# Kernel tuning notes

Hardware: AMD Instinct MI355X
Metric: run time of the kernel (lower is better)

The kernel has to match this reference:

```python
import jax, jax.numpy as jnp
import numpy as np
from math import sqrt

B, S, D_MODEL, H, DK, DV = 8, 1024, 1024, 16, 64, 64
LN_EPS = 1e-5

def setup_inputs() -> dict:
    key = jax.random.key(0)
    ks = jax.random.split(key, 12)
    scale = 1.0 / sqrt(D_MODEL)
    return {
        "input_Q": jax.random.normal(ks[0], (B, S, D_MODEL), jnp.float32),
        "input_K": jax.random.normal(ks[1], (B, S, D_MODEL), jnp.float32),
        "input_V": jax.random.normal(ks[2], (B, S, D_MODEL), jnp.float32),
        "attn_mask": jax.random.randint(ks[3], (B, S, S), 0, 2).astype(bool),
        "matrix": jax.random.uniform(ks[4], (B, 1, S, S), jnp.float32),
        "Wq": jax.random.normal(ks[5], (D_MODEL, H * DK), jnp.float32) * scale,
        "Wk": jax.random.normal(ks[6], (D_MODEL, H * DK), jnp.float32) * scale,
        "Wv": jax.random.normal(ks[7], (D_MODEL, H * DV), jnp.float32) * scale,
        "Wfc": jax.random.normal(ks[8], (H * DV, D_MODEL), jnp.float32) * scale,
        "gamma": jnp.ones((D_MODEL,), jnp.float32),
        "beta": jnp.zeros((D_MODEL,), jnp.float32),
    }

def reference(input_Q, input_K, input_V, attn_mask, matrix, Wq, Wk, Wv, Wfc, gamma, beta):
    b, s, _ = input_Q.shape
    # QKV projections -> [b, h, s, d]
    Q = (input_Q @ Wq).reshape(b, s, H, DK).transpose(0, 2, 1, 3)
    K = (input_K @ Wk).reshape(b, s, H, DK).transpose(0, 2, 1, 3)
    V = (input_V @ Wv).reshape(b, s, H, DV).transpose(0, 2, 1, 3)
    scores = jnp.einsum('bhqd,bhkd->bhqk', Q, K) / sqrt(DK)
    scores = scores * matrix  # custom bias multiply, broadcast over heads
    scores = jnp.where(attn_mask[:, None, :, :], jnp.float32(-1e9), scores)
    attn = jax.nn.softmax(scores, axis=-1)  # dropout p=0 (eval)
    context = jnp.einsum('bhqk,bhkd->bhqd', attn, V)
    context = context.transpose(0, 2, 1, 3).reshape(b, s, H * DV)
    out = context @ Wfc
    mu = jnp.mean(out, axis=-1, keepdims=True)
    var = jnp.var(out, axis=-1, keepdims=True)
    return (out - mu) / jnp.sqrt(var + LN_EPS) * gamma + beta
```

## Files before the change

### kernel.cpp

```cpp
#include <hip/hip_runtime.h>
#include <hip/hip_bf16.h>

typedef __attribute__((ext_vector_type(8))) short short8;
typedef __attribute__((ext_vector_type(4))) float f32x4;

#define NH 16
#define SEQ 1024
#define DMODEL 1024
#define HD 64

__device__ __forceinline__ unsigned short f2bf(float f) {
  unsigned u = __builtin_bit_cast(unsigned, f);
  unsigned r = (u + 0x7FFFu + ((u >> 16) & 1u)) >> 16;
  return (unsigned short)r;
}

__device__ __forceinline__ void gld16(const unsigned short* g, unsigned short* l) {
  __builtin_amdgcn_global_load_lds(
      (const __attribute__((address_space(1))) unsigned int*)g,
      (__attribute__((address_space(3))) unsigned int*)l, 16, 0, 0);
}

__device__ __forceinline__ void stage_tile_gld(const unsigned short* __restrict__ gtile,
                                               unsigned short* ldsbuf, int w, int l) {
#pragma unroll
  for (int it = 0; it < 2; ++it) {
    int e = (w * 2 + it) * 512 + l * 8;
    int row = e >> 5, col = e & 31;
    gld16(gtile + (size_t)row * 1024 + col, ldsbuf + e);
  }
}

__global__ void mask_detect(const unsigned char* __restrict__ mask,
                            int* __restrict__ flag) {
  __shared__ int cA, cB;
  if (threadIdx.x == 0) { cA = 0; cB = 0; }
  __syncthreads();
  int a = 0, b = 0;
  for (int i = threadIdx.x; i < 4096; i += 256) {
    unsigned char v = mask[i];
    if (v) { if ((i & 3) == 0) a = 1; else b = 1; }
  }
  if (a) atomicOr(&cA, 1);
  if (b) atomicOr(&cB, 1);
  __syncthreads();
  if (threadIdx.x == 0) flag[0] = cA ? (cB ? 0 : 1) : 2;
}

__device__ __forceinline__ unsigned nib_of(int mmode,
    const unsigned char* __restrict__ mask, const int* __restrict__ maski,
    const float* __restrict__ maskf, size_t eoff) {
  if (mmode == 0) {
    unsigned mu = *(const unsigned*)(mask + eoff);
    return ((mu & 0xFFu) ? 1u : 0u) | ((mu & 0xFF00u) ? 2u : 0u) |
           ((mu & 0xFF0000u) ? 4u : 0u) | ((mu & 0xFF000000u) ? 8u : 0u);
  } else if (mmode == 1) {
    int4 m4 = *(const int4*)(maski + eoff);
    return (m4.x ? 1u : 0u) | (m4.y ? 2u : 0u) | (m4.z ? 4u : 0u) | (m4.w ? 8u : 0u);
  } else {
    float4 m4 = *(const float4*)(maskf + eoff);
    return (m4.x != 0.f ? 1u : 0u) | (m4.y != 0.f ? 2u : 0u) |
           (m4.z != 0.f ? 4u : 0u) | (m4.w != 0.f ? 8u : 0u);
  }
}

__global__ __launch_bounds__(256) void wtrans_kernel(
    const float* __restrict__ W0, const float* __restrict__ W1,
    const float* __restrict__ W2, const float* __restrict__ W3,
    unsigned short* __restrict__ out) {
  int z = blockIdx.z;
  const float* W = (z == 0) ? W0 : (z == 1) ? W1 : (z == 2) ? W2 : W3;
  unsigned short* o = out + (size_t)z * DMODEL * DMODEL;
  __shared__ float t[32][33];
  int tid = threadIdx.x;
  int tx = tid & 31, ty = tid >> 5;
  int n0 = blockIdx.x * 32, k0 = blockIdx.y * 32;
#pragma unroll
  for (int i = 0; i < 4; ++i)
    t[ty + 8 * i][tx] = W[(size_t)(k0 + ty + 8 * i) * DMODEL + n0 + tx];
  __syncthreads();
#pragma unroll
  for (int i = 0; i < 4; ++i)
    o[(size_t)(n0 + ty + 8 * i) * DMODEL + k0 + tx] = f2bf(t[tx][ty + 8 * i]);
}

__global__ __launch_bounds__(256) void cvt_bf16(
    const float* __restrict__ inQ, const float* __restrict__ inK,
    const float* __restrict__ inV, unsigned short* __restrict__ Abf) {
  int z = blockIdx.y;
  const float* src = (z == 0) ? inQ : (z == 1) ? inK : inV;
  unsigned short* dst = Abf + (size_t)z * 8192 * DMODEL;
  float scale = (z == 0) ? 0.125f : 1.0f;
  size_t i = ((size_t)blockIdx.x * 256 + threadIdx.x) * 8;
  float4 v0 = *(const float4*)&src[i];
  float4 v1 = *(const float4*)&src[i + 4];
  short8 r;
  r[0] = (short)f2bf(v0.x * scale); r[1] = (short)f2bf(v0.y * scale);
  r[2] = (short)f2bf(v0.z * scale); r[3] = (short)f2bf(v0.w * scale);
  r[4] = (short)f2bf(v1.x * scale); r[5] = (short)f2bf(v1.y * scale);
  r[6] = (short)f2bf(v1.z * scale); r[7] = (short)f2bf(v1.w * scale);
  *(short8*)&dst[i] = r;
}

__device__ __forceinline__ size_t kf_idx(int bh, int s, int d) {
  int kt = s >> 6, sl = s & 63;
  int lane = ((d >> 3) & 3) * 16 + (sl & 15);
  return ((size_t)bh * 16 + kt) * 4096 + ((((d >> 5) << 2) + (sl >> 4)) << 9) + lane * 8 + (d & 7);
}
__device__ __forceinline__ size_t vf_idx(int bh, int s, int d) {
  int kt = s >> 6, sl = s & 63;
  int lane = ((sl >> 3) & 3) * 16 + (d & 15);
  return ((size_t)bh * 16 + kt) * 4096 + ((((sl >> 5) << 2) + (d >> 4)) << 9) + lane * 8 + (sl & 7);
}

__global__ __launch_bounds__(256) void qkv_gemm_bf(
    const unsigned short* __restrict__ Abf, const unsigned short* __restrict__ Wt,
    unsigned short* __restrict__ Qp, unsigned short* __restrict__ Kf,
    unsigned short* __restrict__ Vf) {
  __shared__ unsigned short As[2][4096];
  __shared__ unsigned short Bs[2][4096];
  int tid = threadIdx.x;
  int which = blockIdx.z;
  const unsigned short* A = Abf + (size_t)which * 8192 * DMODEL;
  const unsigned short* Bt = Wt + (size_t)which * DMODEL * DMODEL;
  int m0 = blockIdx.x * 128, n0 = blockIdx.y * 128;
  int w = tid >> 6, l = tid & 63, lr = l & 15, lh = l >> 4;
  int wr = (w >> 1) * 64, wc = (w & 1) * 64;

  f32x4 acc[4][4];
#pragma unroll
  for (int i = 0; i < 4; ++i)
#pragma unroll
    for (int j = 0; j < 4; ++j) acc[i][j] = (f32x4){0.f, 0.f, 0.f, 0.f};

  const unsigned short* Abase = A + (size_t)m0 * DMODEL;
  const unsigned short* Bbase = Bt + (size_t)n0 * DMODEL;

  stage_tile_gld(Abase, As[0], w, l);
  stage_tile_gld(Bbase, Bs[0], w, l);
  __syncthreads();

  for (int kt = 0; kt < 32; ++kt) {
    int buf = kt & 1;
    if (kt < 31) {
      stage_tile_gld(Abase + (kt + 1) * 32, As[buf ^ 1], w, l);
      stage_tile_gld(Bbase + (kt + 1) * 32, Bs[buf ^ 1], w, l);
    }
    short8 a[4], b[4];
#pragma unroll
    for (int i = 0; i < 4; ++i) a[i] = *(const short8*)&As[buf][(wr + i * 16 + lr) * 32 + lh * 8];
#pragma unroll
    for (int i = 0; i < 4; ++i) b[i] = *(const short8*)&Bs[buf][(wc + i * 16 + lr) * 32 + lh * 8];
#pragma unroll
    for (int mi = 0; mi < 4; ++mi)
#pragma unroll
      for (int ni = 0; ni < 4; ++ni)
        acc[mi][ni] = __builtin_amdgcn_mfma_f32_16x16x32_bf16(a[mi], b[ni], acc[mi][ni], 0, 0, 0);
    __syncthreads();
  }

#pragma unroll
  for (int mi = 0; mi < 4; ++mi)
#pragma unroll
    for (int ni = 0; ni < 4; ++ni)
#pragma unroll
      for (int r = 0; r < 4; ++r) {
        int m = m0 + wr + mi * 16 + lh * 4 + r;
        int n = n0 + wc + ni * 16 + lr;
        int bb = m >> 10, s = m & 1023, hh = n >> 6, d = n & 63;
        int bh = bb * NH + hh;
        unsigned short val = f2bf(acc[mi][ni][r]);
        if (which == 0)      Qp[((size_t)bh * SEQ + s) * HD + d] = val;
        else if (which == 1) Kf[kf_idx(bh, s, d)] = val;
        else                 Vf[vf_idx(bh, s, d)] = val;
      }
}

__global__ __launch_bounds__(256) void qkv_gemm_legacy(
    const float* __restrict__ inQ, const float* __restrict__ inK,
    const float* __restrict__ inV, const unsigned short* __restrict__ Wt,
    unsigned short* __restrict__ Qp, unsigned short* __restrict__ Kf,
    unsigned short* __restrict__ Vf) {
  __shared__ unsigned short As[2][128][40];
  __shared__ unsigned short Bs[2][128][40];
  int tid = threadIdx.x;
  int which = blockIdx.z;
  const float* A = (which == 0) ? inQ : (which == 1) ? inK : inV;
  const unsigned short* Bt = Wt + (size_t)which * DMODEL * DMODEL;
  float scale = (which == 0) ? 0.125f : 1.0f;
  int m0 = blockIdx.x * 128, n0 = blockIdx.y * 128;
  int w = tid >> 6, l = tid & 63, lr = l & 15, lh = l >> 4;
  int wr = (w >> 1) * 64, wc = (w & 1) * 64;

  f32x4 acc[4][4];
#pragma unroll
  for (int i = 0; i < 4; ++i)
#pragma unroll
    for (int j = 0; j < 4; ++j) acc[i][j] = (f32x4){0.f, 0.f, 0.f, 0.f};

  const float* Abase = A + (size_t)m0 * DMODEL;
  const unsigned short* Bbase = Bt + (size_t)n0 * DMODEL;

  {
    int row = tid >> 1, seg = (tid & 1) << 4;
    const float4* p = (const float4*)(Abase + (size_t)row * DMODEL + seg);
    float4 v0 = p[0], v1 = p[1], v2 = p[2], v3 = p[3];
    short8 r0, r1;
    r0[0] = (short)f2bf(v0.x); r0[1] = (short)f2bf(v0.y);
    r0[2] = (short)f2bf(v0.z); r0[3] = (short)f2bf(v0.w);
    r0[4] = (short)f2bf(v1.x); r0[5] = (short)f2bf(v1.y);
    r0[6] = (short)f2bf(v1.z); r0[7] = (short)f2bf(v1.w);
    r1[0] = (short)f2bf(v2.x); r1[1] = (short)f2bf(v2.y);
    r1[2] = (short)f2bf(v2.z); r1[3] = (short)f2bf(v2.w);
    r1[4] = (short)f2bf(v3.x); r1[5] = (short)f2bf(v3.y);
    r1[6] = (short)f2bf(v3.z); r1[7] = (short)f2bf(v3.w);
    *(short8*)&As[0][row][seg] = r0;
    *(short8*)&As[0][row][seg + 8] = r1;
    const short8* pb = (const short8*)(Bbase + (size_t)row * DMODEL + seg);
    *(short8*)&Bs[0][row][seg] = pb[0];
    *(short8*)&Bs[0][row][seg + 8] = pb[1];
  }
  __syncthreads();

  for (int kt = 0; kt < 32; ++kt) {
    int buf = kt & 1;
    if (kt < 31) {
      int row = tid >> 1, seg = (tid & 1) << 4;
      const float4* p = (const float4*)(Abase + (kt + 1) * 32 + (size_t)row * DMODEL + seg);
      float4 v0 = p[0], v1 = p[1], v2 = p[2], v3 = p[3];
      short8 r0, r1;
      r0[0] = (short)f2bf(v0.x); r0[1] = (short)f2bf(v0.y);
      r0[2] = (short)f2bf(v0.z); r0[3] = (short)f2bf(v0.w);
      r0[4] = (short)f2bf(v1.x); r0[5] = (short)f2bf(v1.y);
      r0[6] = (short)f2bf(v1.z); r0[7] = (short)f2bf(v1.w);
      r1[0] = (short)f2bf(v2.x); r1[1] = (short)f2bf(v2.y);
      r1[2] = (short)f2bf(v2.z); r1[3] = (short)f2bf(v2.w);
      r1[4] = (short)f2bf(v3.x); r1[5] = (short)f2bf(v3.y);
      r1[6] = (short)f2bf(v3.z); r1[7] = (short)f2bf(v3.w);
      *(short8*)&As[buf ^ 1][row][seg] = r0;
      *(short8*)&As[buf ^ 1][row][seg + 8] = r1;
      const short8* pb = (const short8*)(Bbase + (kt + 1) * 32 + (size_t)row * DMODEL + seg);
      *(short8*)&Bs[buf ^ 1][row][seg] = pb[0];
      *(short8*)&Bs[buf ^ 1][row][seg + 8] = pb[1];
    }
    short8 a[4], b[4];
#pragma unroll
    for (int i = 0; i < 4; ++i) a[i] = *(const short8*)&As[buf][wr + i * 16 + lr][lh * 8];
#pragma unroll
    for (int i = 0; i < 4; ++i) b[i] = *(const short8*)&Bs[buf][wc + i * 16 + lr][lh * 8];
#pragma unroll
    for (int mi = 0; mi < 4; ++mi)
#pragma unroll
      for (int ni = 0; ni < 4; ++ni)
        acc[mi][ni] = __builtin_amdgcn_mfma_f32_16x16x32_bf16(a[mi], b[ni], acc[mi][ni], 0, 0, 0);
    __syncthreads();
  }

#pragma unroll
  for (int mi = 0; mi < 4; ++mi)
#pragma unroll
    for (int ni = 0; ni < 4; ++ni)
#pragma unroll
      for (int r = 0; r < 4; ++r) {
        int m = m0 + wr + mi * 16 + lh * 4 + r;
        int n = n0 + wc + ni * 16 + lr;
        int bb = m >> 10, s = m & 1023, hh = n >> 6, d = n & 63;
        int bh = bb * NH + hh;
        unsigned short val = f2bf(acc[mi][ni][r] * scale);
        if (which == 0)      Qp[((size_t)bh * SEQ + s) * HD + d] = val;
        else if (which == 1) Kf[kf_idx(bh, s, d)] = val;
        else                 Vf[vf_idx(bh, s, d)] = val;
      }
}

__global__ __launch_bounds__(512, 2) void attn_kernel(
    const unsigned short* __restrict__ Qp, const unsigned short* __restrict__ Kf,
    const unsigned short* __restrict__ Vf, const float* __restrict__ matrix,
    const unsigned char* __restrict__ mask, const int* __restrict__ maskmode,
    unsigned short* __restrict__ ctx) {
  __shared__ float Msc[2][32][68];
  __shared__ float Msb[2][32][68];
  __shared__ unsigned short Ps[8][16][72];

  int tid = threadIdx.x, w = tid >> 6, l = tid & 63, lr = l & 15, lh = l >> 4;
  int id = blockIdx.x;
  int b = id & 7;
  int rest = id >> 3;
  int qt = rest & 31, pass = rest >> 5;
  int q0 = qt * 32;
  int h = pass * 8 + w;
  int mmode = maskmode[0];
  const int* maski = (const int*)mask;
  const float* maskf = (const float*)mask;

  int srow = tid >> 4, sf4 = tid & 15;
  size_t mrow = ((size_t)b * SEQ + q0 + srow) * SEQ;

  int bh = b * NH + h;
  const unsigned short* Qb = Qp + (size_t)bh * SEQ * HD;
  size_t fb = (size_t)bh * 16 * 4096;

  short8 aq[2][2];
#pragma unroll
  for (int qs = 0; qs < 2; ++qs)
#pragma unroll
    for (int kd = 0; kd < 2; ++kd)
      aq[qs][kd] = *(const short8*)&Qb[(size_t)(q0 + qs * 16 + lr) * HD + kd * 32 + lh * 8];

  float lrun[2] = {0.f, 0.f};
  f32x4 cacc[2][4];
#pragma unroll
  for (int qs = 0; qs < 2; ++qs)
#pragma unroll
    for (int di = 0; di < 4; ++di) cacc[qs][di] = (f32x4){0.f, 0.f, 0.f, 0.f};

  {
    size_t eoff = mrow + sf4 * 4;
    float4 m0v = *(const float4*)&matrix[eoff];
    unsigned nb = nib_of(mmode, mask, maski, maskf, eoff);
    float4 sv, bsv;
    sv.x = (nb & 1u) ? 0.f : m0v.x;  bsv.x = (nb & 1u) ? -30000.f : -12.f;
    sv.y = (nb & 2u) ? 0.f : m0v.y;  bsv.y = (nb & 2u) ? -30000.f : -12.f;
    sv.z = (nb & 4u) ? 0.f : m0v.z;  bsv.z = (nb & 4u) ? -30000.f : -12.f;
    sv.w = (nb & 8u) ? 0.f : m0v.w;  bsv.w = (nb & 8u) ? -30000.f : -12.f;
    *(float4*)&Msc[0][srow][sf4 * 4] = sv;
    *(float4*)&Msb[0][srow][sf4 * 4] = bsv;
  }
  __syncthreads();

  int cur = 0;
  for (int kt = 0; kt < 16; ++kt) {
    float4 mpre = {0.f, 0.f, 0.f, 0.f};
    unsigned npre = 0;
    if (kt < 15) {
      size_t eoff = mrow + kt * 64 + 64 + sf4 * 4;
      mpre = *(const float4*)&matrix[eoff];
      npre = nib_of(mmode, mask, maski, maskf, eoff);
    }
    size_t ktb = fb + (size_t)kt * 4096;
    short8 bk[4][2], bv[4][2];
#pragma unroll
    for (int ni = 0; ni < 4; ++ni)
#pragma unroll
      for (int kd = 0; kd < 2; ++kd)
        bk[ni][kd] = *(const short8*)&Kf[ktb + (((kd << 2) + ni) << 9) + (l << 3)];
#pragma unroll
    for (int di = 0; di < 4; ++di)
#pragma unroll
      for (int kd = 0; kd < 2; ++kd)
        bv[di][kd] = *(const short8*)&Vf[ktb + (((kd << 2) + di) << 9) + (l << 3)];

#pragma unroll
    for (int qs = 0; qs < 2; ++qs) {
      f32x4 sc[4];
#pragma unroll
      for (int ni = 0; ni < 4; ++ni) sc[ni] = (f32x4){0.f, 0.f, 0.f, 0.f};
#pragma unroll
      for (int ni = 0; ni < 4; ++ni)
#pragma unroll
        for (int kd = 0; kd < 2; ++kd)
          sc[ni] = __builtin_amdgcn_mfma_f32_16x16x32_bf16(bk[ni][kd], aq[qs][kd], sc[ni], 0, 0, 0);
      int qrw = qs * 16 + lr;
      float psum = 0.f;
#pragma unroll
      for (int ni = 0; ni < 4; ++ni) {
        float4 sa = *(const float4*)&Msc[cur][qrw][(ni * 4 + lh) * 4];
        float4 sb = *(const float4*)&Msb[cur][qrw][(ni * 4 + lh) * 4];
        float p0 = __expf(sc[ni][0] * sa.x + sb.x);
        float p1 = __expf(sc[ni][1] * sa.y + sb.y);
        float p2 = __expf(sc[ni][2] * sa.z + sb.z);
        float p3 = __expf(sc[ni][3] * sa.w + sb.w);
        psum += (p0 + p1) + (p2 + p3);
        Ps[w][lr][ni * 16 + lh * 4 + 0] = f2bf(p0);
        Ps[w][lr][ni * 16 + lh * 4 + 1] = f2bf(p1);
        Ps[w][lr][ni * 16 + lh * 4 + 2] = f2bf(p2);
        Ps[w][lr][ni * 16 + lh * 4 + 3] = f2bf(p3);
      }
      lrun[qs] += psum;
      short8 ap[2];
#pragma unroll
      for (int kd = 0; kd < 2; ++kd)
        ap[kd] = *(const short8*)&Ps[w][lr][kd * 32 + lh * 8];
#pragma unroll
      for (int di = 0; di < 4; ++di)
#pragma unroll
        for (int kd = 0; kd < 2; ++kd)
          cacc[qs][di] = __builtin_amdgcn_mfma_f32_16x16x32_bf16(ap[kd], bv[di][kd], cacc[qs][di], 0, 0, 0);
    }
    if (kt < 15) {
      float4 sv, bsv;
      sv.x = (npre & 1u) ? 0.f : mpre.x;  bsv.x = (npre & 1u) ? -30000.f : -12.f;
      sv.y = (npre & 2u) ? 0.f : mpre.y;  bsv.y = (npre & 2u) ? -30000.f : -12.f;
      sv.z = (npre & 4u) ? 0.f : mpre.z;  bsv.z = (npre & 4u) ? -30000.f : -12.f;
      sv.w = (npre & 8u) ? 0.f : mpre.w;  bsv.w = (npre & 8u) ? -30000.f : -12.f;
      *(float4*)&Msc[cur ^ 1][srow][sf4 * 4] = sv;
      *(float4*)&Msb[cur ^ 1][srow][sf4 * 4] = bsv;
    }
    __syncthreads();
    cur ^= 1;
  }

#pragma unroll
  for (int qs = 0; qs < 2; ++qs) {
    float l2 = lrun[qs];
    l2 += __shfl_xor(l2, 16);
    l2 += __shfl_xor(l2, 32);
    float ls[4];
    int cbase = lh * 4;
#pragma unroll
    for (int r = 0; r < 4; ++r) ls[r] = __shfl(l2, cbase + r);
#pragma unroll
    for (int di = 0; di < 4; ++di)
#pragma unroll
      for (int r = 0; r < 4; ++r) {
        int q = q0 + qs * 16 + lh * 4 + r;
        int col = h * HD + di * 16 + lr;
        ctx[((size_t)b * SEQ + q) * DMODEL + col] = f2bf(cacc[qs][di][r] / ls[r]);
      }
  }
}

__global__ __launch_bounds__(256) void fc_gemm(
    const unsigned short* __restrict__ Actx, const unsigned short* __restrict__ Bt,
    float* __restrict__ Cout) {
  __shared__ unsigned short As[2][4096];
  __shared__ unsigned short Bs[2][4096];
  int tid = threadIdx.x;
  int m0 = blockIdx.x * 128, n0 = blockIdx.y * 128;
  int w = tid >> 6, l = tid & 63, lr = l & 15, lh = l >> 4;
  int wr = (w >> 1) * 64, wc = (w & 1) * 64;

  f32x4 acc[4][4];
#pragma unroll
  for (int i = 0; i < 4; ++i)
#pragma unroll
    for (int j = 0; j < 4; ++j) acc[i][j] = (f32x4){0.f, 0.f, 0.f, 0.f};

  const unsigned short* Abase = Actx + (size_t)m0 * DMODEL;
  const unsigned short* Bbase = Bt + (size_t)n0 * DMODEL;

  stage_tile_gld(Abase, As[0], w, l);
  stage_tile_gld(Bbase, Bs[0], w, l);
  __syncthreads();

  for (int kt = 0; kt < 32; ++kt) {
    int buf = kt & 1;
    if (kt < 31) {
      stage_tile_gld(Abase + (kt + 1) * 32, As[buf ^ 1], w, l);
      stage_tile_gld(Bbase + (kt + 1) * 32, Bs[buf ^ 1], w, l);
    }
    short8 a[4], b[4];
#pragma unroll
    for (int i = 0; i < 4; ++i) a[i] = *(const short8*)&As[buf][(wr + i * 16 + lr) * 32 + lh * 8];
#pragma unroll
    for (int i = 0; i < 4; ++i) b[i] = *(const short8*)&Bs[buf][(wc + i * 16 + lr) * 32 + lh * 8];
#pragma unroll
    for (int mi = 0; mi < 4; ++mi)
#pragma unroll
      for (int ni = 0; ni < 4; ++ni)
        acc[mi][ni] = __builtin_amdgcn_mfma_f32_16x16x32_bf16(a[mi], b[ni], acc[mi][ni], 0, 0, 0);
    __syncthreads();
  }

#pragma unroll
  for (int mi = 0; mi < 4; ++mi)
#pragma unroll
    for (int ni = 0; ni < 4; ++ni)
#pragma unroll
      for (int r = 0; r < 4; ++r) {
        int m = m0 + wr + mi * 16 + lh * 4 + r;
        int n = n0 + wc + ni * 16 + lr;
        Cout[(size_t)m * DMODEL + n] = acc[mi][ni][r];
      }
}

__global__ __launch_bounds__(256) void ln_kernel(
    const float* __restrict__ x, const float* __restrict__ gamma,
    const float* __restrict__ beta, float* __restrict__ out) {
  int row = blockIdx.x, tid = threadIdx.x;
  const float* xr = x + (size_t)row * DMODEL;
  float4 v = *(const float4*)&xr[tid * 4];
  float s = v.x + v.y + v.z + v.w;
  float s2 = v.x * v.x + v.y * v.y + v.z * v.z + v.w * v.w;
#pragma unroll
  for (int mm = 1; mm < 64; mm <<= 1) {
    s += __shfl_xor(s, mm);
    s2 += __shfl_xor(s2, mm);
  }
  __shared__ float red[8];
  int w = tid >> 6, l = tid & 63;
  if (l == 0) { red[w] = s; red[4 + w] = s2; }
  __syncthreads();
  s = red[0] + red[1] + red[2] + red[3];
  s2 = red[4] + red[5] + red[6] + red[7];
  float mu = s * (1.0f / 1024.0f);
  float var = s2 * (1.0f / 1024.0f) - mu * mu;
  float rstd = rsqrtf(var + 1e-5f);
  float4 g = *(const float4*)&gamma[tid * 4];
  float4 be = *(const float4*)&beta[tid * 4];
  float4 o;
  o.x = (v.x - mu) * rstd * g.x + be.x;
  o.y = (v.y - mu) * rstd * g.y + be.y;
  o.z = (v.z - mu) * rstd * g.z + be.z;
  o.w = (v.w - mu) * rstd * g.w + be.w;
  *(float4*)(out + (size_t)row * DMODEL + tid * 4) = o;
}

extern "C" void kernel_launch(void* const* d_in, const int* in_sizes, int n_in,
                              void* d_out, int out_size, void* d_ws, size_t ws_size,
                              hipStream_t stream) {
  const float* inQ = (const float*)d_in[0];
  const float* inK = (const float*)d_in[1];
  const float* inV = (const float*)d_in[2];
  const unsigned char* mask = (const unsigned char*)d_in[3];
  const float* matrix = (const float*)d_in[4];
  const float* Wq = (const float*)d_in[5];
  const float* Wk = (const float*)d_in[6];
  const float* Wv = (const float*)d_in[7];
  const float* Wfc = (const float*)d_in[8];
  const float* gamma = (const float*)d_in[9];
  const float* beta = (const float*)d_in[10];
  float* out = (float*)d_out;

  char* ws = (char*)d_ws;
  const size_t MB = 1024 * 1024;
  unsigned short* Wt = (unsigned short*)(ws);
  unsigned short* Qp = (unsigned short*)(ws + 8 * MB);
  unsigned short* Kf = (unsigned short*)(ws + 24 * MB);
  unsigned short* Vf = (unsigned short*)(ws + 40 * MB);
  unsigned short* ctx = (unsigned short*)(ws + 56 * MB);
  unsigned short* Abf = (unsigned short*)(ws + 72 * MB);
  float* fcout = (float*)(ws + 8 * MB);
  int* maskflag = (int*)(ws + ((ws_size - 64) & ~(size_t)63));

  bool big_ws = ws_size >= 121 * MB;

  mask_detect<<<1, 256, 0, stream>>>(mask, maskflag);
  wtrans_kernel<<<dim3(32, 32, 4), 256, 0, stream>>>(Wq, Wk, Wv, Wfc, Wt);
  if (big_ws) {
    cvt_bf16<<<dim3(4096, 3), 256, 0, stream>>>(inQ, inK, inV, Abf);
    qkv_gemm_bf<<<dim3(64, 8, 3), 256, 0, stream>>>(Abf, Wt, Qp, Kf, Vf);
  } else {
    qkv_gemm_legacy<<<dim3(64, 8, 3), 256, 0, stream>>>(inQ, inK, inV, Wt, Qp, Kf, Vf);
  }
  attn_kernel<<<dim3(512), 512, 0, stream>>>(Qp, Kf, Vf, matrix, mask, maskflag, ctx);
  fc_gemm<<<dim3(64, 8), 256, 0, stream>>>(ctx, Wt + (size_t)3 * 1024 * 1024, fcout);
  ln_kernel<<<8192, 256, 0, stream>>>(fcout, gamma, beta, out);
}
```

Baseline: 258.7 us.

## Fuse fp32-to-bf16 input conversion into QKV GEMM with register-staged prefetch

Removes the separate cvt_bf16 pass and its bf16 workspace buffer. The QKV GEMM now reads fp32 activations directly into registers, converts and scales them, and writes them to LDS after the MFMA block so the global loads overlap compute. The B tile uses direct global-to-LDS loads. This removes one full read and write of the activations, in exchange for doubling A-tile global traffic inside the GEMM and extra VALU conversion work.

```diff
diff --git a/kernel.cpp b/kernel.cpp
--- a/kernel.cpp
+++ b/kernel.cpp
@@ -28,6 +28,26 @@
     int e = (w * 2 + it) * 512 + l * 8;
     int row = e >> 5, col = e & 31;
     gld16(gtile + (size_t)row * 1024 + col, ldsbuf + e);
+  }
+}
+
+__device__ __forceinline__ void stage_a_load(const float* __restrict__ Ab, int kt,
+                                             int t, float4 va[4]) {
+#pragma unroll
+  for (int j = 0; j < 4; ++j) {
+    int row = j * 32 + (t >> 3), col = (t & 7) * 4;
+    va[j] = *(const float4*)&Ab[(size_t)row * DMODEL + kt * 32 + col];
+  }
+}
+__device__ __forceinline__ void stage_a_write(unsigned short* dst, int t,
+                                              const float4 va[4], float scale) {
+#pragma unroll
+  for (int j = 0; j < 4; ++j) {
+    int row = j * 32 + (t >> 3), col = (t & 7) * 4;
+    unsigned w0 = (unsigned)f2bf(va[j].x * scale) | ((unsigned)f2bf(va[j].y * scale) << 16);
+    unsigned w1 = (unsigned)f2bf(va[j].z * scale) | ((unsigned)f2bf(va[j].w * scale) << 16);
+    *(unsigned*)&dst[row * 32 + col] = w0;
+    *(unsigned*)&dst[row * 32 + col + 2] = w1;
   }
 }
 
@@ -84,24 +104,6 @@
     o[(size_t)(n0 + ty + 8 * i) * DMODEL + k0 + tx] = f2bf(t[tx][ty + 8 * i]);
 }
 
-__global__ __launch_bounds__(256) void cvt_bf16(
-    const float* __restrict__ inQ, const float* __restrict__ inK,
-    const float* __restrict__ inV, unsigned short* __restrict__ Abf) {
-  int z = blockIdx.y;
-  const float* src = (z == 0) ? inQ : (z == 1) ? inK : inV;
-  unsigned short* dst = Abf + (size_t)z * 8192 * DMODEL;
-  float scale = (z == 0) ? 0.125f : 1.0f;
-  size_t i = ((size_t)blockIdx.x * 256 + threadIdx.x) * 8;
-  float4 v0 = *(const float4*)&src[i];
-  float4 v1 = *(const float4*)&src[i + 4];
-  short8 r;
-  r[0] = (short)f2bf(v0.x * scale); r[1] = (short)f2bf(v0.y * scale);
-  r[2] = (short)f2bf(v0.z * scale); r[3] = (short)f2bf(v0.w * scale);
-  r[4] = (short)f2bf(v1.x * scale); r[5] = (short)f2bf(v1.y * scale);
-  r[6] = (short)f2bf(v1.z * scale); r[7] = (short)f2bf(v1.w * scale);
-  *(short8*)&dst[i] = r;
-}
-
 __device__ __forceinline__ size_t kf_idx(int bh, int s, int d) {
   int kt = s >> 6, sl = s & 63;
   int lane = ((d >> 3) & 3) * 16 + (sl & 15);
@@ -113,76 +115,13 @@
   return ((size_t)bh * 16 + kt) * 4096 + ((((sl >> 5) << 2) + (d >> 4)) << 9) + lane * 8 + (sl & 7);
 }
 
-__global__ __launch_bounds__(256) void qkv_gemm_bf(
-    const unsigned short* __restrict__ Abf, const unsigned short* __restrict__ Wt,
+__global__ __launch_bounds__(256) void qkv_gemm_f32a(
+    const float* __restrict__ inQ, const float* __restrict__ inK,
+    const float* __restrict__ inV, const unsigned short* __restrict__ Wt,
     unsigned short* __restrict__ Qp, unsigned short* __restrict__ Kf,
     unsigned short* __restrict__ Vf) {
   __shared__ unsigned short As[2][4096];
   __shared__ unsigned short Bs[2][4096];
-  int tid = threadIdx.x;
-  int which = blockIdx.z;
-  const unsigned short* A = Abf + (size_t)which * 8192 * DMODEL;
-  const unsigned short* Bt = Wt + (size_t)which * DMODEL * DMODEL;
-  int m0 = blockIdx.x * 128, n0 = blockIdx.y * 128;
-  int w = tid >> 6, l = tid & 63, lr = l & 15, lh = l >> 4;
-  int wr = (w >> 1) * 64, wc = (w & 1) * 64;
-
-  f32x4 acc[4][4];
-#pragma unroll
-  for (int i = 0; i < 4; ++i)
-#pragma unroll
-    for (int j = 0; j < 4; ++j) acc[i][j] = (f32x4){0.f, 0.f, 0.f, 0.f};
-
-  const unsigned short* Abase = A + (size_t)m0 * DMODEL;
-  const unsigned short* Bbase = Bt + (size_t)n0 * DMODEL;
-
-  stage_tile_gld(Abase, As[0], w, l);
-  stage_tile_gld(Bbase, Bs[0], w, l);
-  __syncthreads();
-
-  for (int kt = 0; kt < 32; ++kt) {
-    int buf = kt & 1;
-    if (kt < 31) {
-      stage_tile_gld(Abase + (kt + 1) * 32, As[buf ^ 1], w, l);
-      stage_tile_gld(Bbase + (kt + 1) * 32, Bs[buf ^ 1], w, l);
-    }
-    short8 a[4], b[4];
-#pragma unroll
-    for (int i = 0; i < 4; ++i) a[i] = *(const short8*)&As[buf][(wr + i * 16 + lr) * 32 + lh * 8];
-#pragma unroll
-    for (int i = 0; i < 4; ++i) b[i] = *(const short8*)&Bs[buf][(wc + i * 16 + lr) * 32 + lh * 8];
-#pragma unroll
-    for (int mi = 0; mi < 4; ++mi)
-#pragma unroll
-      for (int ni = 0; ni < 4; ++ni)
-        acc[mi][ni] = __builtin_amdgcn_mfma_f32_16x16x32_bf16(a[mi], b[ni], acc[mi][ni], 0, 0, 0);
-    __syncthreads();
-  }
-
-#pragma unroll
-  for (int mi = 0; mi < 4; ++mi)
-#pragma unroll
-    for (int ni = 0; ni < 4; ++ni)
-#pragma unroll
-      for (int r = 0; r < 4; ++r) {
-        int m = m0 + wr + mi * 16 + lh * 4 + r;
-        int n = n0 + wc + ni * 16 + lr;
-        int bb = m >> 10, s = m & 1023, hh = n >> 6, d = n & 63;
-        int bh = bb * NH + hh;
-        unsigned short val = f2bf(acc[mi][ni][r]);
-        if (which == 0)      Qp[((size_t)bh * SEQ + s) * HD + d] = val;
-        else if (which == 1) Kf[kf_idx(bh, s, d)] = val;
-        else                 Vf[vf_idx(bh, s, d)] = val;
-      }
-}
-
-__global__ __launch_bounds__(256) void qkv_gemm_legacy(
-    const float* __restrict__ inQ, const float* __restrict__ inK,
-    const float* __restrict__ inV, const unsigned short* __restrict__ Wt,
-    unsigned short* __restrict__ Qp, unsigned short* __restrict__ Kf,
-    unsigned short* __restrict__ Vf) {
-  __shared__ unsigned short As[2][128][40];
-  __shared__ unsigned short Bs[2][128][40];
   int tid = threadIdx.x;
   int which = blockIdx.z;
   const float* A = (which == 0) ? inQ : (which == 1) ? inK : inV;
@@ -202,57 +141,31 @@
   const unsigned short* Bbase = Bt + (size_t)n0 * DMODEL;
 
   {
-    int row = tid >> 1, seg = (tid & 1) << 4;
-    const float4* p = (const float4*)(Abase + (size_t)row * DMODEL + seg);
-    float4 v0 = p[0], v1 = p[1], v2 = p[2], v3 = p[3];
-    short8 r0, r1;
-    r0[0] = (short)f2bf(v0.x); r0[1] = (short)f2bf(v0.y);
-    r0[2] = (short)f2bf(v0.z); r0[3] = (short)f2bf(v0.w);
-    r0[4] = (short)f2bf(v1.x); r0[5] = (short)f2bf(v1.y);
-    r0[6] = (short)f2bf(v1.z); r0[7] = (short)f2bf(v1.w);
-    r1[0] = (short)f2bf(v2.x); r1[1] = (short)f2bf(v2.y);
-    r1[2] = (short)f2bf(v2.z); r1[3] = (short)f2bf(v2.w);
-    r1[4] = (short)f2bf(v3.x); r1[5] = (short)f2bf(v3.y);
-    r1[6] = (short)f2bf(v3.z); r1[7] = (short)f2bf(v3.w);
-    *(short8*)&As[0][row][seg] = r0;
-    *(short8*)&As[0][row][seg + 8] = r1;
-    const short8* pb = (const short8*)(Bbase + (size_t)row * DMODEL + seg);
-    *(short8*)&Bs[0][row][seg] = pb[0];
-    *(short8*)&Bs[0][row][seg + 8] = pb[1];
+    float4 va[4];
+    stage_a_load(Abase, 0, tid, va);
+    stage_a_write(As[0], tid, va, scale);
+    stage_tile_gld(Bbase, Bs[0], w, l);
   }
   __syncthreads();
 
   for (int kt = 0; kt < 32; ++kt) {
     int buf = kt & 1;
+    float4 va[4];
     if (kt < 31) {
-      int row = tid >> 1, seg = (tid & 1) << 4;
-      const float4* p = (const float4*)(Abase + (kt + 1) * 32 + (size_t)row * DMODEL + seg);
-      float4 v0 = p[0], v1 = p[1], v2 = p[2], v3 = p[3];
-      short8 r0, r1;
-      r0[0] = (short)f2bf(v0.x); r0[1] = (short)f2bf(v0.y);
-      r0[2] = (short)f2bf(v0.z); r0[3] = (short)f2bf(v0.w);
-      r0[4] = (short)f2bf(v1.x); r0[5] = (short)f2bf(v1.y);
-      r0[6] = (short)f2bf(v1.z); r0[7] = (short)f2bf(v1.w);
-      r1[0] = (short)f2bf(v2.x); r1[1] = (short)f2bf(v2.y);
-      r1[2] = (short)f2bf(v2.z); r1[3] = (short)f2bf(v2.w);
-      r1[4] = (short)f2bf(v3.x); r1[5] = (short)f2bf(v3.y);
-      r1[6] = (short)f2bf(v3.z); r1[7] = (short)f2bf(v3.w);
-      *(short8*)&As[buf ^ 1][row][seg] = r0;
-      *(short8*)&As[buf ^ 1][row][seg + 8] = r1;
-      const short8* pb = (const short8*)(Bbase + (kt + 1) * 32 + (size_t)row * DMODEL + seg);
-      *(short8*)&Bs[buf ^ 1][row][seg] = pb[0];
-      *(short8*)&Bs[buf ^ 1][row][seg + 8] = pb[1];
+      stage_a_load(Abase, kt + 1, tid, va);
+      stage_tile_gld(Bbase + (kt + 1) * 32, Bs[buf ^ 1], w, l);
     }
     short8 a[4], b[4];
 #pragma unroll
-    for (int i = 0; i < 4; ++i) a[i] = *(const short8*)&As[buf][wr + i * 16 + lr][lh * 8];
-#pragma unroll
-    for (int i = 0; i < 4; ++i) b[i] = *(const short8*)&Bs[buf][wc + i * 16 + lr][lh * 8];
+    for (int i = 0; i < 4; ++i) a[i] = *(const short8*)&As[buf][(wr + i * 16 + lr) * 32 + lh * 8];
+#pragma unroll
+    for (int i = 0; i < 4; ++i) b[i] = *(const short8*)&Bs[buf][(wc + i * 16 + lr) * 32 + lh * 8];
 #pragma unroll
     for (int mi = 0; mi < 4; ++mi)
 #pragma unroll
       for (int ni = 0; ni < 4; ++ni)
         acc[mi][ni] = __builtin_amdgcn_mfma_f32_16x16x32_bf16(a[mi], b[ni], acc[mi][ni], 0, 0, 0);
+    if (kt < 31) stage_a_write(As[buf ^ 1], tid, va, scale);
     __syncthreads();
   }
 
@@ -266,7 +179,7 @@
         int n = n0 + wc + ni * 16 + lr;
         int bb = m >> 10, s = m & 1023, hh = n >> 6, d = n & 63;
         int bh = bb * NH + hh;
-        unsigned short val = f2bf(acc[mi][ni][r] * scale);
+        unsigned short val = f2bf(acc[mi][ni][r]);
         if (which == 0)      Qp[((size_t)bh * SEQ + s) * HD + d] = val;
         else if (which == 1) Kf[kf_idx(bh, s, d)] = val;
         else                 Vf[vf_idx(bh, s, d)] = val;
@@ -529,20 +442,12 @@
   unsigned short* Kf = (unsigned short*)(ws + 24 * MB);
   unsigned short* Vf = (unsigned short*)(ws + 40 * MB);
   unsigned short* ctx = (unsigned short*)(ws + 56 * MB);
-  unsigned short* Abf = (unsigned short*)(ws + 72 * MB);
   float* fcout = (float*)(ws + 8 * MB);
   int* maskflag = (int*)(ws + ((ws_size - 64) & ~(size_t)63));
 
-  bool big_ws = ws_size >= 121 * MB;
-
   mask_detect<<<1, 256, 0, stream>>>(mask, maskflag);
   wtrans_kernel<<<dim3(32, 32, 4), 256, 0, stream>>>(Wq, Wk, Wv, Wfc, Wt);
-  if (big_ws) {
-    cvt_bf16<<<dim3(4096, 3), 256, 0, stream>>>(inQ, inK, inV, Abf);
-    qkv_gemm_bf<<<dim3(64, 8, 3), 256, 0, stream>>>(Abf, Wt, Qp, Kf, Vf);
-  } else {
-    qkv_gemm_legacy<<<dim3(64, 8, 3), 256, 0, stream>>>(inQ, inK, inV, Wt, Qp, Kf, Vf);
-  }
+  qkv_gemm_f32a<<<dim3(64, 8, 3), 256, 0, stream>>>(inQ, inK, inV, Wt, Qp, Kf, Vf);
   attn_kernel<<<dim3(512), 512, 0, stream>>>(Qp, Kf, Vf, matrix, mask, maskflag, ctx);
   fc_gemm<<<dim3(64, 8), 256, 0, stream>>>(ctx, Wt + (size_t)3 * 1024 * 1024, fcout);
   ln_kernel<<<8192, 256, 0, stream>>>(fcout, gamma, beta, out);
```

Result: no change. 263.7 us (+1.9%).

## Shrink attention query tile to 16 rows, raise occupancy, store FC output as bf16

Applied to the files above, without the earlier changes.

The attention kernel now handles 16 query rows per block instead of 32, doubling the grid to 1024 blocks. It loads V fragments just in time and raises the launch bound to 4 blocks per CU, aiming for more parallelism and lower register pressure. The price is that K/V tiles are reloaded twice as often. The FC GEMM output is now written as bf16 and upconverted in the LayerNorm kernel, halving that intermediate's traffic at some cost in precision before normalisation.

```diff
diff --git a/kernel.cpp b/kernel.cpp
--- a/kernel.cpp
+++ b/kernel.cpp
@@ -13,6 +13,10 @@
   unsigned u = __builtin_bit_cast(unsigned, f);
   unsigned r = (u + 0x7FFFu + ((u >> 16) & 1u)) >> 16;
   return (unsigned short)r;
+}
+__device__ __forceinline__ float bf2f(unsigned short s) {
+  unsigned u = ((unsigned)s) << 16;
+  return __builtin_bit_cast(float, u);
 }
 
 __device__ __forceinline__ void gld16(const unsigned short* g, unsigned short* l) {
@@ -273,48 +277,45 @@
       }
 }
 
-__global__ __launch_bounds__(512, 2) void attn_kernel(
+__global__ __launch_bounds__(512, 4) void attn_kernel(
     const unsigned short* __restrict__ Qp, const unsigned short* __restrict__ Kf,
     const unsigned short* __restrict__ Vf, const float* __restrict__ matrix,
     const unsigned char* __restrict__ mask, const int* __restrict__ maskmode,
     unsigned short* __restrict__ ctx) {
-  __shared__ float Msc[2][32][68];
-  __shared__ float Msb[2][32][68];
+  __shared__ float Msc[2][16][68];
+  __shared__ float Msb[2][16][68];
   __shared__ unsigned short Ps[8][16][72];
 
   int tid = threadIdx.x, w = tid >> 6, l = tid & 63, lr = l & 15, lh = l >> 4;
   int id = blockIdx.x;
   int b = id & 7;
   int rest = id >> 3;
-  int qt = rest & 31, pass = rest >> 5;
-  int q0 = qt * 32;
+  int qt = rest & 63, pass = rest >> 6;
+  int q0 = qt * 16;
   int h = pass * 8 + w;
   int mmode = maskmode[0];
   const int* maski = (const int*)mask;
   const float* maskf = (const float*)mask;
 
-  int srow = tid >> 4, sf4 = tid & 15;
+  bool stager = tid < 256;
+  int srow = (tid >> 4) & 15, sf4 = tid & 15;
   size_t mrow = ((size_t)b * SEQ + q0 + srow) * SEQ;
 
   int bh = b * NH + h;
   const unsigned short* Qb = Qp + (size_t)bh * SEQ * HD;
   size_t fb = (size_t)bh * 16 * 4096;
 
-  short8 aq[2][2];
-#pragma unroll
-  for (int qs = 0; qs < 2; ++qs)
-#pragma unroll
-    for (int kd = 0; kd < 2; ++kd)
-      aq[qs][kd] = *(const short8*)&Qb[(size_t)(q0 + qs * 16 + lr) * HD + kd * 32 + lh * 8];
-
-  float lrun[2] = {0.f, 0.f};
-  f32x4 cacc[2][4];
-#pragma unroll
-  for (int qs = 0; qs < 2; ++qs)
-#pragma unroll
-    for (int di = 0; di < 4; ++di) cacc[qs][di] = (f32x4){0.f, 0.f, 0.f, 0.f};
-
-  {
+  short8 aq[2];
+#pragma unroll
+  for (int kd = 0; kd < 2; ++kd)
+    aq[kd] = *(const short8*)&Qb[(size_t)(q0 + lr) * HD + kd * 32 + lh * 8];
+
+  float lrun = 0.f;
+  f32x4 cacc[4];
+#pragma unroll
+  for (int di = 0; di < 4; ++di) cacc[di] = (f32x4){0.f, 0.f, 0.f, 0.f};
+
+  if (stager) {
     size_t eoff = mrow + sf4 * 4;
     float4 m0v = *(const float4*)&matrix[eoff];
     unsigned nb = nib_of(mmode, mask, maski, maskf, eoff);
@@ -332,62 +333,55 @@
   for (int kt = 0; kt < 16; ++kt) {
     float4 mpre = {0.f, 0.f, 0.f, 0.f};
     unsigned npre = 0;
-    if (kt < 15) {
+    if (stager && kt < 15) {
       size_t eoff = mrow + kt * 64 + 64 + sf4 * 4;
       mpre = *(const float4*)&matrix[eoff];
       npre = nib_of(mmode, mask, maski, maskf, eoff);
     }
     size_t ktb = fb + (size_t)kt * 4096;
-    short8 bk[4][2], bv[4][2];
+    short8 bk[4][2];
 #pragma unroll
     for (int ni = 0; ni < 4; ++ni)
 #pragma unroll
       for (int kd = 0; kd < 2; ++kd)
         bk[ni][kd] = *(const short8*)&Kf[ktb + (((kd << 2) + ni) << 9) + (l << 3)];
-#pragma unroll
-    for (int di = 0; di < 4; ++di)
+
+    f32x4 sc[4];
+#pragma unroll
+    for (int ni = 0; ni < 4; ++ni) sc[ni] = (f32x4){0.f, 0.f, 0.f, 0.f};
+#pragma unroll
+    for (int ni = 0; ni < 4; ++ni)
 #pragma unroll
       for (int kd = 0; kd < 2; ++kd)
-        bv[di][kd] = *(const short8*)&Vf[ktb + (((kd << 2) + di) << 9) + (l << 3)];
-
-#pragma unroll
-    for (int qs = 0; qs < 2; ++qs) {
-      f32x4 sc[4];
-#pragma unroll
-      for (int ni = 0; ni < 4; ++ni) sc[ni] = (f32x4){0.f, 0.f, 0.f, 0.f};
-#pragma unroll
-      for (int ni = 0; ni < 4; ++ni)
-#pragma unroll
-        for (int kd = 0; kd < 2; ++kd)
-          sc[ni] = __builtin_amdgcn_mfma_f32_16x16x32_bf16(bk[ni][kd], aq[qs][kd], sc[ni], 0, 0, 0);
-      int qrw = qs * 16 + lr;
-      float psum = 0.f;
-#pragma unroll
-      for (int ni = 0; ni < 4; ++ni) {
-        float4 sa = *(const float4*)&Msc[cur][qrw][(ni * 4 + lh) * 4];
-        float4 sb = *(const float4*)&Msb[cur][qrw][(ni * 4 + lh) * 4];
-        float p0 = __expf(sc[ni][0] * sa.x + sb.x);
-        float p1 = __expf(sc[ni][1] * sa.y + sb.y);
-        float p2 = __expf(sc[ni][2] * sa.z + sb.z);
-        float p3 = __expf(sc[ni][3] * sa.w + sb.w);
-        psum += (p0 + p1) + (p2 + p3);
-        Ps[w][lr][ni * 16 + lh * 4 + 0] = f2bf(p0);
-        Ps[w][lr][ni * 16 + lh * 4 + 1] = f2bf(p1);
-        Ps[w][lr][ni * 16 + lh * 4 + 2] = f2bf(p2);
-        Ps[w][lr][ni * 16 + lh * 4 + 3] = f2bf(p3);
-      }
-      lrun[qs] += psum;
-      short8 ap[2];
-#pragma unroll
-      for (int kd = 0; kd < 2; ++kd)
-        ap[kd] = *(const short8*)&Ps[w][lr][kd * 32 + lh * 8];
-#pragma unroll
-      for (int di = 0; di < 4; ++di)
-#pragma unroll
-        for (int kd = 0; kd < 2; ++kd)
-          cacc[qs][di] = __builtin_amdgcn_mfma_f32_16x16x32_bf16(ap[kd], bv[di][kd], cacc[qs][di], 0, 0, 0);
-    }
-    if (kt < 15) {
+        sc[ni] = __builtin_amdgcn_mfma_f32_16x16x32_bf16(bk[ni][kd], aq[kd], sc[ni], 0, 0, 0);
+    float psum = 0.f;
+#pragma unroll
+    for (int ni = 0; ni < 4; ++ni) {
+      float4 sa = *(const float4*)&Msc[cur][lr][(ni * 4 + lh) * 4];
+      float4 sb = *(const float4*)&Msb[cur][lr][(ni * 4 + lh) * 4];
+      float p0 = __expf(sc[ni][0] * sa.x + sb.x);
+      float p1 = __expf(sc[ni][1] * sa.y + sb.y);
+      float p2 = __expf(sc[ni][2] * sa.z + sb.z);
+      float p3 = __expf(sc[ni][3] * sa.w + sb.w);
+      psum += (p0 + p1) + (p2 + p3);
+      Ps[w][lr][ni * 16 + lh * 4 + 0] = f2bf(p0);
+      Ps[w][lr][ni * 16 + lh * 4 + 1] = f2bf(p1);
+      Ps[w][lr][ni * 16 + lh * 4 + 2] = f2bf(p2);
+      Ps[w][lr][ni * 16 + lh * 4 + 3] = f2bf(p3);
+    }
+    lrun += psum;
+    short8 ap[2];
+#pragma unroll
+    for (int kd = 0; kd < 2; ++kd)
+      ap[kd] = *(const short8*)&Ps[w][lr][kd * 32 + lh * 8];
+#pragma unroll
+    for (int di = 0; di < 4; ++di) {
+      short8 bv0 = *(const short8*)&Vf[ktb + (((0 << 2) + di) << 9) + (l << 3)];
+      short8 bv1 = *(const short8*)&Vf[ktb + (((1 << 2) + di) << 9) + (l << 3)];
+      cacc[di] = __builtin_amdgcn_mfma_f32_16x16x32_bf16(ap[0], bv0, cacc[di], 0, 0, 0);
+      cacc[di] = __builtin_amdgcn_mfma_f32_16x16x32_bf16(ap[1], bv1, cacc[di], 0, 0, 0);
+    }
+    if (stager && kt < 15) {
       float4 sv, bsv;
       sv.x = (npre & 1u) ? 0.f : mpre.x;  bsv.x = (npre & 1u) ? -30000.f : -12.f;
       sv.y = (npre & 2u) ? 0.f : mpre.y;  bsv.y = (npre & 2u) ? -30000.f : -12.f;
@@ -400,9 +394,8 @@
     cur ^= 1;
   }
 
-#pragma unroll
-  for (int qs = 0; qs < 2; ++qs) {
-    float l2 = lrun[qs];
+  {
+    float l2 = lrun;
     l2 += __shfl_xor(l2, 16);
     l2 += __shfl_xor(l2, 32);
     float ls[4];
@@ -413,16 +406,16 @@
     for (int di = 0; di < 4; ++di)
 #pragma unroll
       for (int r = 0; r < 4; ++r) {
-        int q = q0 + qs * 16 + lh * 4 + r;
+        int q = q0 + lh * 4 + r;
         int col = h * HD + di * 16 + lr;
-        ctx[((size_t)b * SEQ + q) * DMODEL + col] = f2bf(cacc[qs][di][r] / ls[r]);
+        ctx[((size_t)b * SEQ + q) * DMODEL + col] = f2bf(cacc[di][r] / ls[r]);
       }
   }
 }
 
 __global__ __launch_bounds__(256) void fc_gemm(
     const unsigned short* __restrict__ Actx, const unsigned short* __restrict__ Bt,
-    float* __restrict__ Cout) {
+    unsigned short* __restrict__ Cout) {
   __shared__ unsigned short As[2][4096];
   __shared__ unsigned short Bs[2][4096];
   int tid = threadIdx.x;
@@ -470,16 +463,18 @@
       for (int r = 0; r < 4; ++r) {
         int m = m0 + wr + mi * 16 + lh * 4 + r;
         int n = n0 + wc + ni * 16 + lr;
-        Cout[(size_t)m * DMODEL + n] = acc[mi][ni][r];
+        Cout[(size_t)m * DMODEL + n] = f2bf(acc[mi][ni][r]);
       }
 }
 
 __global__ __launch_bounds__(256) void ln_kernel(
-    const float* __restrict__ x, const float* __restrict__ gamma,
+    const unsigned short* __restrict__ x, const float* __restrict__ gamma,
     const float* __restrict__ beta, float* __restrict__ out) {
   int row = blockIdx.x, tid = threadIdx.x;
-  const float* xr = x + (size_t)row * DMODEL;
-  float4 v = *(const float4*)&xr[tid * 4];
+  const unsigned short* xr = x + (size_t)row * DMODEL;
+  ushort4 uv = *(const ushort4*)&xr[tid * 4];
+  float4 v;
+  v.x = bf2f(uv.x); v.y = bf2f(uv.y); v.z = bf2f(uv.z); v.w = bf2f(uv.w);
   float s = v.x + v.y + v.z + v.w;
   float s2 = v.x * v.x + v.y * v.y + v.z * v.z + v.w * v.w;
 #pragma unroll
@@ -530,7 +525,7 @@
   unsigned short* Vf = (unsigned short*)(ws + 40 * MB);
   unsigned short* ctx = (unsigned short*)(ws + 56 * MB);
   unsigned short* Abf = (unsigned short*)(ws + 72 * MB);
-  float* fcout = (float*)(ws + 8 * MB);
+  unsigned short* fcout = (unsigned short*)(ws + 8 * MB);
   int* maskflag = (int*)(ws + ((ws_size - 64) & ~(size_t)63));
 
   bool big_ws = ws_size >= 121 * MB;
@@ -543,7 +538,7 @@
   } else {
     qkv_gemm_legacy<<<dim3(64, 8, 3), 256, 0, stream>>>(inQ, inK, inV, Wt, Qp, Kf, Vf);
   }
-  attn_kernel<<<dim3(512), 512, 0, stream>>>(Qp, Kf, Vf, matrix, mask, maskflag, ctx);
+  attn_kernel<<<dim3(1024), 512, 0, stream>>>(Qp, Kf, Vf, matrix, mask, maskflag, ctx);
   fc_gemm<<<dim3(64, 8), 256, 0, stream>>>(ctx, Wt + (size_t)3 * 1024 * 1024, fcout);
   ln_kernel<<<8192, 256, 0, stream>>>(fcout, gamma, beta, out);
 }
```

Measured after the change: 247.4 us. -4.4%, faster.
